# Performance work log

Hardware: AMD Instinct MI355X
Metric: run time of the kernel (lower is better)

## Reference

```python
import jax, jax.numpy as jnp
import numpy as np
import math

N_SLOTS, DIM, ITERS = 8, 256, 3
BATCH, TOKENS = 64, 4096


def _ln(x, g, b, eps=1e-5):
    mu = x.mean(-1, keepdims=True)
    var = ((x - mu) ** 2).mean(-1, keepdims=True)
    return (x - mu) * jax.lax.rsqrt(var + eps) * g + b


def setup_inputs() -> dict:
    key = jax.random.key(0)
    ks = jax.random.split(key, 16)
    d = DIM
    s = 0.02
    return {
        "inputs": jax.random.normal(ks[0], (BATCH, TOKENS, d), jnp.float32),
        "noise": jax.random.normal(ks[1], (BATCH, N_SLOTS, d), jnp.float32),
        "slots_mu": jax.random.normal(ks[2], (1, N_SLOTS, d), jnp.float32),
        "slots_logsigma": jnp.zeros((1, N_SLOTS, d), jnp.float32),
        "Wq": jax.random.normal(ks[3], (d, d), jnp.float32) * s,
        "Wk": jax.random.normal(ks[4], (d, d), jnp.float32) * s,
        "Wv": jax.random.normal(ks[5], (d, d), jnp.float32) * s,
        "W_ih": jax.random.normal(ks[6], (3 * d, d), jnp.float32) * s,
        "W_hh": jax.random.normal(ks[7], (3 * d, d), jnp.float32) * s,
        "b_ih": jnp.zeros((3 * d,), jnp.float32),
        "b_hh": jnp.zeros((3 * d,), jnp.float32),
        "mlp_W1": jax.random.normal(ks[8], (d, d), jnp.float32) * s,
        "mlp_b1": jnp.zeros((d,), jnp.float32),
        "mlp_W2": jax.random.normal(ks[9], (d, d), jnp.float32) * s,
        "mlp_b2": jnp.zeros((d,), jnp.float32),
        "ln_in_g": jnp.ones((d,), jnp.float32),
        "ln_in_b": jnp.zeros((d,), jnp.float32),
        "ln_slots_g": jnp.ones((d,), jnp.float32),
        "ln_slots_b": jnp.zeros((d,), jnp.float32),
        "ln_mlp_g": jnp.ones((d,), jnp.float32),
        "ln_mlp_b": jnp.zeros((d,), jnp.float32),
    }


def reference(inputs, noise, slots_mu, slots_logsigma, Wq, Wk, Wv,
              W_ih, W_hh, b_ih, b_hh, mlp_W1, mlp_b1, mlp_W2, mlp_b2,
              ln_in_g, ln_in_b, ln_slots_g, ln_slots_b, ln_mlp_g, ln_mlp_b):
    n, t, d = inputs.shape
    scale = 1.0 / math.sqrt(d)
    x = _ln(inputs, ln_in_g, ln_in_b)                      # [n,t,d]
    slots = slots_mu + jnp.exp(slots_logsigma) * noise     # [n,S,d]
    k = jnp.einsum('ntd,ed->nte', x, Wk)
    v = jnp.einsum('ntd,ed->nte', x, Wv)
    for _ in range(ITERS):
        slots_prev = slots
        q = jnp.einsum('nsd,ed->nse', _ln(slots, ln_slots_g, ln_slots_b), Wq)
        logits = jnp.einsum('nsd,ntd->nst', q, k) * scale  # [n,S,t]
        attn = jax.nn.softmax(logits, axis=-1)
        attn = attn / (attn.sum(-1, keepdims=True) + 1e-8)
        updates = jnp.einsum('nst,ntd->nsd', attn, v)      # [n,S,d]
        # GRUCell (torch gate order r,z,n)
        gi = jnp.einsum('nsd,ed->nse', updates, W_ih) + b_ih
        gh = jnp.einsum('nsd,ed->nse', slots_prev, W_hh) + b_hh
        gi_r, gi_z, gi_n = jnp.split(gi, 3, axis=-1)
        gh_r, gh_z, gh_n = jnp.split(gh, 3, axis=-1)
        r = jax.nn.sigmoid(gi_r + gh_r)
        z = jax.nn.sigmoid(gi_z + gh_z)
        h_new = jnp.tanh(gi_n + r * gh_n)
        slots = (1.0 - z) * h_new + z * slots_prev
        hid = jax.nn.relu(jnp.einsum('nsd,ed->nse', _ln(slots, ln_mlp_g, ln_mlp_b), mlp_W1) + mlp_b1)
        slots = slots + jnp.einsum('nsd,ed->nse', hid, mlp_W2) + mlp_b2
    return slots
```

## Files before the change

kernel.cpp:

```cpp
#include <hip/hip_runtime.h>
#include <math.h>

#define TOKENS 4096
#define BATCH 64

typedef __attribute__((ext_vector_type(8))) short bf16x8;
typedef __attribute__((ext_vector_type(4))) float f32x4;
union U4B { uint4 u; bf16x8 b; };
union U2x2B { uint2 u[2]; bf16x8 b; };

__device__ __forceinline__ float wsum(float v) {
#pragma unroll
  for (int m = 32; m >= 1; m >>= 1) v += __shfl_xor(v, m);
  return v;
}
__device__ __forceinline__ unsigned short f2bf(float f) {
  unsigned u = __float_as_uint(f);
  u += 0x7fffu + ((u >> 16) & 1u);
  return (unsigned short)(u >> 16);
}
__device__ __forceinline__ float bflo(unsigned p) { return __uint_as_float(p << 16); }
__device__ __forceinline__ float bfhi(unsigned p) { return __uint_as_float(p & 0xffff0000u); }
__device__ __forceinline__ float sigmf(float x) { return 1.f / (1.f + expf(-x)); }

__global__ __launch_bounds__(256) void k_pre(
    const float* __restrict__ in, const float* __restrict__ lin_g,
    const float* __restrict__ lin_b, unsigned* __restrict__ x,
    const float* __restrict__ Wq, const float* __restrict__ Wv,
    const float* __restrict__ Wih, const float* __restrict__ Whh,
    const float* __restrict__ W1, const float* __restrict__ W2,
    float* __restrict__ WqT, float* __restrict__ WvT, float* __restrict__ WihT,
    float* __restrict__ WhhT, float* __restrict__ W1T, float* __restrict__ W2T) {
  int bid = blockIdx.x, tid = threadIdx.x;
  if (bid < 65536) {
    int row = bid * 4 + (tid >> 6);
    int lane = tid & 63;
    const float* p = in + (size_t)row * 256 + lane * 4;
    float4 v = *(const float4*)p;
    float s  = wsum(v.x + v.y + v.z + v.w);
    float sq = wsum(v.x * v.x + v.y * v.y + v.z * v.z + v.w * v.w);
    float mu = s * (1.f / 256.f);
    float var = sq * (1.f / 256.f) - mu * mu;
    float rs = rsqrtf(var + 1e-5f);
    float4 gg = *(const float4*)(lin_g + lane * 4);
    float4 bb = *(const float4*)(lin_b + lane * 4);
    float y0 = (v.x - mu) * rs * gg.x + bb.x;
    float y1 = (v.y - mu) * rs * gg.y + bb.y;
    float y2 = (v.z - mu) * rs * gg.z + bb.z;
    float y3 = (v.w - mu) * rs * gg.w + bb.w;
    uint2 o;
    o.x = (unsigned)f2bf(y0) | ((unsigned)f2bf(y1) << 16);
    o.y = (unsigned)f2bf(y2) | ((unsigned)f2bf(y3) << 16);
    *(uint2*)(x + (size_t)row * 128 + lane * 2) = o;
    return;
  }
  {
    __shared__ float t[32][33];
    int t2 = bid - 65536;
    const float* S; float* D; int R; int tile;
    if (t2 < 64)       { S = Wq;  D = WqT;  R = 256; tile = t2; }
    else if (t2 < 128) { S = Wv;  D = WvT;  R = 256; tile = t2 - 64; }
    else if (t2 < 192) { S = W1;  D = W1T;  R = 256; tile = t2 - 128; }
    else if (t2 < 256) { S = W2;  D = W2T;  R = 256; tile = t2 - 192; }
    else if (t2 < 448) { S = Wih; D = WihT; R = 768; tile = t2 - 256; }
    else               { S = Whh; D = WhhT; R = 768; tile = t2 - 448; }
    int rt = R >> 5;
    int r0 = (tile % rt) * 32, c0 = (tile / rt) * 32;
    int ci = tid & 31, r8 = tid >> 5;
#pragma unroll
    for (int k = 0; k < 4; ++k) {
      int r = r8 + k * 8;
      t[r][ci] = S[(size_t)(r0 + r) * 256 + c0 + ci];
    }
    __syncthreads();
#pragma unroll
    for (int k = 0; k < 4; ++k) {
      int r = r8 + k * 8;
      D[(size_t)(c0 + r) * R + r0 + ci] = t[ci][r];
    }
  }
}

__global__ __launch_bounds__(256) void k_qw0(
    const float* __restrict__ smu, const float* __restrict__ slsig,
    const float* __restrict__ noise, const float* __restrict__ lsl_g,
    const float* __restrict__ lsl_b, const float* __restrict__ WqT,
    const float* __restrict__ Wk, float* __restrict__ slots,
    unsigned* __restrict__ qwb) {
  __shared__ float ln[256];
  __shared__ float q[256];
  __shared__ float red[8];
  int n = blockIdx.x, s = blockIdx.y, tid = threadIdx.x;
  int sd = s * 256 + tid;
  float v = smu[sd] + expf(slsig[sd]) * noise[(size_t)n * 2048 + sd];
  slots[(size_t)n * 2048 + sd] = v;
  float ps = wsum(v), pq = wsum(v * v);
  if ((tid & 63) == 0) { red[tid >> 6] = ps; red[4 + (tid >> 6)] = pq; }
  __syncthreads();
  float sum = red[0] + red[1] + red[2] + red[3];
  float sqq = red[4] + red[5] + red[6] + red[7];
  float mu = sum * (1.f / 256.f);
  float var = sqq * (1.f / 256.f) - mu * mu;
  float rs = rsqrtf(var + 1e-5f);
  ln[tid] = (v - mu) * rs * lsl_g[tid] + lsl_b[tid];
  __syncthreads();
  float a = 0.f;
  for (int d = 0; d < 256; ++d) a += ln[d] * WqT[d * 256 + tid];
  q[tid] = a;
  __syncthreads();
  float c = 0.f;
  for (int e = 0; e < 256; ++e) c += q[e] * Wk[(size_t)e * 256 + tid];
  c *= 0.0625f;
  __syncthreads();
  ln[tid] = c;
  __syncthreads();
  if (tid < 128)
    qwb[((size_t)n * 8 + s) * 128 + tid] =
        (unsigned)f2bf(ln[2 * tid]) | ((unsigned)f2bf(ln[2 * tid + 1]) << 16);
}

__global__ __launch_bounds__(256) void k_att(const unsigned* __restrict__ x,
                                             const unsigned* __restrict__ qwb,
                                             float2* __restrict__ stats,
                                             float* __restrict__ axp) {
  __shared__ unsigned xs[64][130];
  __shared__ float lsT[64][8];
  __shared__ float redM[8][4], redS[8][4];
  int ch = blockIdx.x, n = blockIdx.y;
  int tid = threadIdx.x, wv = tid >> 6, l = tid & 63;
  int col = l & 15, g = l >> 4;
  {
    int lane32 = tid & 31, g8 = tid >> 5;
    const unsigned* src = x + ((size_t)n * 4096 + ch * 64) * 128 + lane32 * 4;
#pragma unroll
    for (int p = 0; p < 8; ++p) {
      int row = p * 8 + g8;
      uint4 vv = *(const uint4*)(src + (size_t)row * 128);
      unsigned* dr = &xs[row][lane32 * 4];
      *(uint2*)dr = make_uint2(vv.x, vv.y);
      *(uint2*)(dr + 2) = make_uint2(vv.z, vv.w);
    }
  }
  uint4 a[8];
  {
    const unsigned* ap = qwb + ((size_t)n * 8 + (l & 7)) * 128 + g * 4;
#pragma unroll
    for (int kk = 0; kk < 8; ++kk) a[kk] = *(const uint4*)(ap + kk * 16);
  }
  __syncthreads();
  {
    int t0 = wv * 16;
    const unsigned* xr = &xs[t0 + col][0];
    f32x4 acc = {0.f, 0.f, 0.f, 0.f};
#pragma unroll
    for (int kk = 0; kk < 8; ++kk) {
      U4B aa;
      aa.u = a[kk];
      U2x2B bb;
      bb.u[0] = *(const uint2*)(xr + kk * 16 + g * 4);
      bb.u[1] = *(const uint2*)(xr + kk * 16 + g * 4 + 2);
      acc = __builtin_amdgcn_mfma_f32_16x16x32_bf16(aa.b, bb.b, acc, 0, 0, 0);
    }
    if (g < 2) {
#pragma unroll
      for (int r = 0; r < 4; ++r) lsT[t0 + col][g * 4 + r] = acc[r];
    }
  }
  __syncthreads();
  int s = tid & 7, tg = tid >> 3;
  float l0 = lsT[tg][s], l1 = lsT[tg + 32][s];
  {
    float M = fmaxf(l0, l1);
    M = fmaxf(M, __shfl_xor(M, 8));
    M = fmaxf(M, __shfl_xor(M, 16));
    M = fmaxf(M, __shfl_xor(M, 32));
    if ((tid & 63) < 8) redM[s][tid >> 6] = M;
  }
  __syncthreads();
  float Mf = fmaxf(fmaxf(redM[s][0], redM[s][1]), fmaxf(redM[s][2], redM[s][3]));
  {
    float e0 = expf(l0 - Mf), e1 = expf(l1 - Mf);
    lsT[tg][s] = e0;
    lsT[tg + 32][s] = e1;
    float S = e0 + e1;
    S += __shfl_xor(S, 8);
    S += __shfl_xor(S, 16);
    S += __shfl_xor(S, 32);
    if ((tid & 63) < 8) redS[s][tid >> 6] = S;
  }
  __syncthreads();
  if (tid < 8) {
    float M = fmaxf(fmaxf(redM[tid][0], redM[tid][1]), fmaxf(redM[tid][2], redM[tid][3]));
    float S = redS[tid][0] + redS[tid][1] + redS[tid][2] + redS[tid][3];
    stats[((size_t)n * 8 + tid) * 64 + ch] = make_float2(M, S);
  }
  {
    int d = tid;
    float acc[8] = {0, 0, 0, 0, 0, 0, 0, 0};
#pragma unroll 8
    for (int t = 0; t < 64; ++t) {
      unsigned pw = xs[t][d >> 1];
      float xv = (d & 1) ? bfhi(pw) : bflo(pw);
      float4 a0 = *(const float4*)&lsT[t][0];
      float4 a1 = *(const float4*)&lsT[t][4];
      acc[0] += a0.x * xv; acc[1] += a0.y * xv;
      acc[2] += a0.z * xv; acc[3] += a0.w * xv;
      acc[4] += a1.x * xv; acc[5] += a1.y * xv;
      acc[6] += a1.z * xv; acc[7] += a1.w * xv;
    }
    float* op = axp + (((size_t)n * 64 + ch) * 8) * 256 + d;
#pragma unroll
    for (int ss = 0; ss < 8; ++ss) op[ss * 256] = acc[ss];
  }
}

__global__ __launch_bounds__(512) void k_update3(
    const float* __restrict__ axp, const float2* __restrict__ stats,
    const float* __restrict__ slots_in,
    const float* __restrict__ WvT, const float* __restrict__ WihT,
    const float* __restrict__ WhhT, const float* __restrict__ b_ih,
    const float* __restrict__ b_hh, const float* __restrict__ W1T,
    const float* __restrict__ b1, const float* __restrict__ W2T,
    const float* __restrict__ b2, const float* __restrict__ lml_g,
    const float* __restrict__ lml_b, const float* __restrict__ lsl_g,
    const float* __restrict__ lsl_b, const float* __restrict__ WqT,
    const float* __restrict__ Wk, unsigned* __restrict__ qwb, int doQw,
    float* __restrict__ slots_out) {
  __shared__ float ax[4][256];
  __shared__ float sp[4][256];
  __shared__ float upd[4][256];
  __shared__ float gi[4][768];
  __shared__ float gh[4][768];
  __shared__ float sn[4][256];
  __shared__ float lnv[4][256];
  __shared__ float hid[4][256];
  __shared__ float red[16];
  __shared__ float wch[4][64];
  __shared__ float inv4[4];
  int n = blockIdx.x, sg = blockIdx.y * 4;
  int tid = threadIdx.x;
  if (tid < 4) {
    const float2* st = stats + ((size_t)n * 8 + sg + tid) * 64;
    float M = -3.4e38f;
#pragma unroll
    for (int c = 0; c < 64; ++c) M = fmaxf(M, st[c].x);
    float S = 0.f;
#pragma unroll
    for (int c = 0; c < 64; ++c) {
      float w = expf(st[c].x - M);
      wch[tid][c] = w;
      S += w * st[c].y;
    }
    inv4[tid] = 1.f / (S * (1.f + 1e-8f));
  }
  __syncthreads();
  for (int i = tid; i < 1024; i += 512) {
    int sl = i >> 8, d = i & 255;
    const float* pp = axp + ((size_t)n * 512 + sg + sl) * 256 + d;
    float a = 0.f;
#pragma unroll
    for (int c = 0; c < 64; ++c) a += wch[sl][c] * pp[(size_t)c * 2048];
    ax[sl][d] = a * inv4[sl];
    sp[sl][d] = slots_in[((size_t)n * 8 + sg + sl) * 256 + d];
  }
  __syncthreads();
  int e = tid & 255, h = tid >> 8;
  {
    float a0 = 0.f, a1 = 0.f;
    for (int d = 0; d < 256; ++d) {
      float w = WvT[d * 256 + e];
      a0 += ax[h * 2][d] * w;
      a1 += ax[h * 2 + 1][d] * w;
    }
    upd[h * 2][e] = a0;
    upd[h * 2 + 1][e] = a1;
  }
  __syncthreads();
  for (int jj = tid; jj < 1536; jj += 512) {
    bool ihs = jj < 768;
    int j = ihs ? jj : jj - 768;
    const float* WT = ihs ? WihT : WhhT;
    const float* src = ihs ? &upd[0][0] : &sp[0][0];
    float a0 = 0.f, a1 = 0.f, a2 = 0.f, a3 = 0.f;
    for (int d = 0; d < 256; ++d) {
      float w = WT[(size_t)d * 768 + j];
      a0 += src[d] * w;
      a1 += src[256 + d] * w;
      a2 += src[512 + d] * w;
      a3 += src[768 + d] * w;
    }
    float bb = ihs ? b_ih[j] : b_hh[j];
    float* dst = ihs ? &gi[0][0] : &gh[0][0];
    dst[j] = a0 + bb;
    dst[768 + j] = a1 + bb;
    dst[1536 + j] = a2 + bb;
    dst[2304 + j] = a3 + bb;
  }
  __syncthreads();
  for (int i = tid; i < 1024; i += 512) {
    int sl = i >> 8, j = i & 255;
    float r = sigmf(gi[sl][j] + gh[sl][j]);
    float z = sigmf(gi[sl][j + 256] + gh[sl][j + 256]);
    float hh = tanhf(gi[sl][j + 512] + r * gh[sl][j + 512]);
    sn[sl][j] = (1.f - z) * hh + z * sp[sl][j];
  }
  __syncthreads();
  {
    int sl = tid >> 7, qq = tid & 127;
    float v0 = sn[sl][qq], v1 = sn[sl][qq + 128];
    float ps = wsum(v0 + v1);
    float pq = wsum(v0 * v0 + v1 * v1);
    int wid = tid >> 6;
    if ((tid & 63) == 0) { red[wid] = ps; red[8 + wid] = pq; }
    __syncthreads();
    float ssum = red[sl * 2] + red[sl * 2 + 1];
    float sqq  = red[8 + sl * 2] + red[8 + sl * 2 + 1];
    float mu = ssum * (1.f / 256.f);
    float var = sqq * (1.f / 256.f) - mu * mu;
    float rs = rsqrtf(var + 1e-5f);
    lnv[sl][qq]       = (v0 - mu) * rs * lml_g[qq] + lml_b[qq];
    lnv[sl][qq + 128] = (v1 - mu) * rs * lml_g[qq + 128] + lml_b[qq + 128];
  }
  __syncthreads();
  {
    float a0 = 0.f, a1 = 0.f;
    for (int d = 0; d < 256; ++d) {
      float w = W1T[d * 256 + e];
      a0 += lnv[h * 2][d] * w;
      a1 += lnv[h * 2 + 1][d] * w;
    }
    hid[h * 2][e]     = fmaxf(a0 + b1[e], 0.f);
    hid[h * 2 + 1][e] = fmaxf(a1 + b1[e], 0.f);
  }
  __syncthreads();
  {
    float a0 = 0.f, a1 = 0.f;
    for (int d = 0; d < 256; ++d) {
      float w = W2T[d * 256 + e];
      a0 += hid[h * 2][d] * w;
      a1 += hid[h * 2 + 1][d] * w;
    }
    float o0 = sn[h * 2][e] + a0 + b2[e];
    float o1 = sn[h * 2 + 1][e] + a1 + b2[e];
    slots_out[((size_t)n * 8 + sg + h * 2) * 256 + e]     = o0;
    slots_out[((size_t)n * 8 + sg + h * 2 + 1) * 256 + e] = o1;
    ax[h * 2][e] = o0;
    ax[h * 2 + 1][e] = o1;
  }
  if (!doQw) return;
  __syncthreads();
  {
    int sl = tid >> 7, qq = tid & 127;
    float v0 = ax[sl][qq], v1 = ax[sl][qq + 128];
    float ps = wsum(v0 + v1);
    float pq = wsum(v0 * v0 + v1 * v1);
    int wid = tid >> 6;
    if ((tid & 63) == 0) { red[wid] = ps; red[8 + wid] = pq; }
    __syncthreads();
    float ssum = red[sl * 2] + red[sl * 2 + 1];
    float sqq  = red[8 + sl * 2] + red[8 + sl * 2 + 1];
    float mu = ssum * (1.f / 256.f);
    float var = sqq * (1.f / 256.f) - mu * mu;
    float rs = rsqrtf(var + 1e-5f);
    sp[sl][qq]       = (v0 - mu) * rs * lsl_g[qq] + lsl_b[qq];
    sp[sl][qq + 128] = (v1 - mu) * rs * lsl_g[qq + 128] + lsl_b[qq + 128];
  }
  __syncthreads();
  {
    float a0 = 0.f, a1 = 0.f;
    for (int d = 0; d < 256; ++d) {
      float w = WqT[d * 256 + e];
      a0 += sp[h * 2][d] * w;
      a1 += sp[h * 2 + 1][d] * w;
    }
    upd[h * 2][e] = a0;
    upd[h * 2 + 1][e] = a1;
  }
  __syncthreads();
  {
    float c0 = 0.f, c1 = 0.f;
    for (int ee = 0; ee < 256; ++ee) {
      float w = Wk[(size_t)ee * 256 + e];
      c0 += upd[h * 2][ee] * w;
      c1 += upd[h * 2 + 1][ee] * w;
    }
    hid[h * 2][e]     = c0 * 0.0625f;
    hid[h * 2 + 1][e] = c1 * 0.0625f;
  }
  __syncthreads();
  {
    int sl = tid >> 7, p = tid & 127;
    qwb[((size_t)n * 8 + sg + sl) * 128 + p] =
        (unsigned)f2bf(hid[sl][2 * p]) | ((unsigned)f2bf(hid[sl][2 * p + 1]) << 16);
  }
}

extern "C" void kernel_launch(void* const* d_in, const int* in_sizes, int n_in,
                              void* d_out, int out_size, void* d_ws, size_t ws_size,
                              hipStream_t stream) {
  (void)in_sizes; (void)n_in; (void)out_size; (void)ws_size;
  const float* inputs = (const float*)d_in[0];
  const float* noise  = (const float*)d_in[1];
  const float* smu    = (const float*)d_in[2];
  const float* slsig  = (const float*)d_in[3];
  const float* Wq     = (const float*)d_in[4];
  const float* Wk     = (const float*)d_in[5];
  const float* Wv     = (const float*)d_in[6];
  const float* W_ih   = (const float*)d_in[7];
  const float* W_hh   = (const float*)d_in[8];
  const float* b_ih   = (const float*)d_in[9];
  const float* b_hh   = (const float*)d_in[10];
  const float* W1     = (const float*)d_in[11];
  const float* b1     = (const float*)d_in[12];
  const float* W2     = (const float*)d_in[13];
  const float* b2     = (const float*)d_in[14];
  const float* lin_g  = (const float*)d_in[15];
  const float* lin_b  = (const float*)d_in[16];
  const float* lsl_g  = (const float*)d_in[17];
  const float* lsl_b  = (const float*)d_in[18];
  const float* lml_g  = (const float*)d_in[19];
  const float* lml_b  = (const float*)d_in[20];
  float* out = (float*)d_out;
  char* ws = (char*)d_ws;
  unsigned* x    = (unsigned*)(ws + 0);
  unsigned* qwb  = (unsigned*)(ws + 134217728);
  float2* stats  = (float2*)(ws + 134479872);
  float* axp     = (float*)(ws + 134742016);
  float* WqT     = (float*)(ws + 168296448);
  float* WvT     = (float*)(ws + 168558592);
  float* WihT    = (float*)(ws + 168820736);
  float* WhhT    = (float*)(ws + 169607168);
  float* W1T     = (float*)(ws + 170393600);
  float* W2T     = (float*)(ws + 170655744);

  k_pre<<<dim3(66176), 256, 0, stream>>>(inputs, lin_g, lin_b, x,
                                         Wq, Wv, W_ih, W_hh, W1, W2,
                                         WqT, WvT, WihT, WhhT, W1T, W2T);
  k_qw0<<<dim3(BATCH, 8), 256, 0, stream>>>(smu, slsig, noise, lsl_g, lsl_b,
                                            WqT, Wk, out, qwb);
  for (int it = 0; it < 3; ++it) {
    k_att<<<dim3(64, BATCH), 256, 0, stream>>>(x, qwb, stats, axp);
    k_update3<<<dim3(BATCH, 2), 512, 0, stream>>>(
        axp, stats, out, WvT, WihT, WhhT, b_ih, b_hh, W1T, b1, W2T, b2,
        lml_g, lml_b, lsl_g, lsl_b, WqT, Wk, qwb, (it < 2) ? 1 : 0, out);
  }
}
```

Baseline: 463.5 us.

## Process four token chunks per attention block with online softmax and register prefetch

Each attention block now walks 256 tokens in four 64-token chunks instead of one chunk. It keeps a running max and sum per slot, as in online softmax, and prefetches the next chunk into registers while the current one is being computed. This cuts the per-chunk partial outputs and stats by four, which shrinks the axp workspace and the reduction work in k_update3. In exchange there are more barriers per block and only 1024 blocks instead of 4096, which may lower occupancy and latency hiding.

```diff
diff --git a/kernel.cpp b/kernel.cpp
--- a/kernel.cpp
+++ b/kernel.cpp
@@ -126,89 +126,123 @@
   __shared__ unsigned xs[64][130];
   __shared__ float lsT[64][8];
   __shared__ float redM[8][4], redS[8][4];
-  int ch = blockIdx.x, n = blockIdx.y;
+  __shared__ float Mrun[8], Srun[8], scl[8], Mnew[8];
+  int bk = blockIdx.x, n = blockIdx.y;
   int tid = threadIdx.x, wv = tid >> 6, l = tid & 63;
   int col = l & 15, g = l >> 4;
-  {
-    int lane32 = tid & 31, g8 = tid >> 5;
-    const unsigned* src = x + ((size_t)n * 4096 + ch * 64) * 128 + lane32 * 4;
-#pragma unroll
-    for (int p = 0; p < 8; ++p) {
-      int row = p * 8 + g8;
-      uint4 vv = *(const uint4*)(src + (size_t)row * 128);
-      unsigned* dr = &xs[row][lane32 * 4];
-      *(uint2*)dr = make_uint2(vv.x, vv.y);
-      *(uint2*)(dr + 2) = make_uint2(vv.z, vv.w);
-    }
-  }
   uint4 a[8];
   {
     const unsigned* ap = qwb + ((size_t)n * 8 + (l & 7)) * 128 + g * 4;
 #pragma unroll
     for (int kk = 0; kk < 8; ++kk) a[kk] = *(const uint4*)(ap + kk * 16);
   }
-  __syncthreads();
-  {
-    int t0 = wv * 16;
-    const unsigned* xr = &xs[t0 + col][0];
-    f32x4 acc = {0.f, 0.f, 0.f, 0.f};
-#pragma unroll
-    for (int kk = 0; kk < 8; ++kk) {
-      U4B aa;
-      aa.u = a[kk];
-      U2x2B bb;
-      bb.u[0] = *(const uint2*)(xr + kk * 16 + g * 4);
-      bb.u[1] = *(const uint2*)(xr + kk * 16 + g * 4 + 2);
-      acc = __builtin_amdgcn_mfma_f32_16x16x32_bf16(aa.b, bb.b, acc, 0, 0, 0);
-    }
-    if (g < 2) {
-#pragma unroll
-      for (int r = 0; r < 4; ++r) lsT[t0 + col][g * 4 + r] = acc[r];
-    }
+  if (tid < 8) { Mrun[tid] = -3.4e38f; Srun[tid] = 0.f; }
+  float acc[8] = {0, 0, 0, 0, 0, 0, 0, 0};
+  int lane32 = tid & 31, g8 = tid >> 5;
+  const unsigned* base = x + ((size_t)n * 4096 + bk * 256) * 128 + lane32 * 4;
+  uint4 st[8];
+#pragma unroll
+  for (int p = 0; p < 8; ++p)
+    st[p] = *(const uint4*)(base + (size_t)(p * 8 + g8) * 128);
+#pragma unroll
+  for (int p = 0; p < 8; ++p) {
+    unsigned* dr = &xs[p * 8 + g8][lane32 * 4];
+    *(uint2*)dr = make_uint2(st[p].x, st[p].y);
+    *(uint2*)(dr + 2) = make_uint2(st[p].z, st[p].w);
   }
   __syncthreads();
   int s = tid & 7, tg = tid >> 3;
-  float l0 = lsT[tg][s], l1 = lsT[tg + 32][s];
-  {
-    float M = fmaxf(l0, l1);
-    M = fmaxf(M, __shfl_xor(M, 8));
-    M = fmaxf(M, __shfl_xor(M, 16));
-    M = fmaxf(M, __shfl_xor(M, 32));
-    if ((tid & 63) < 8) redM[s][tid >> 6] = M;
-  }
-  __syncthreads();
-  float Mf = fmaxf(fmaxf(redM[s][0], redM[s][1]), fmaxf(redM[s][2], redM[s][3]));
-  {
-    float e0 = expf(l0 - Mf), e1 = expf(l1 - Mf);
-    lsT[tg][s] = e0;
-    lsT[tg + 32][s] = e1;
-    float S = e0 + e1;
-    S += __shfl_xor(S, 8);
-    S += __shfl_xor(S, 16);
-    S += __shfl_xor(S, 32);
-    if ((tid & 63) < 8) redS[s][tid >> 6] = S;
-  }
-  __syncthreads();
-  if (tid < 8) {
-    float M = fmaxf(fmaxf(redM[tid][0], redM[tid][1]), fmaxf(redM[tid][2], redM[tid][3]));
-    float S = redS[tid][0] + redS[tid][1] + redS[tid][2] + redS[tid][3];
-    stats[((size_t)n * 8 + tid) * 64 + ch] = make_float2(M, S);
-  }
-  {
-    int d = tid;
-    float acc[8] = {0, 0, 0, 0, 0, 0, 0, 0};
+  for (int c = 0; c < 4; ++c) {
+    if (c < 3) {
+      const unsigned* src = base + (size_t)(c + 1) * 64 * 128;
+#pragma unroll
+      for (int p = 0; p < 8; ++p)
+        st[p] = *(const uint4*)(src + (size_t)(p * 8 + g8) * 128);
+    }
+    {
+      int t0 = wv * 16;
+      const unsigned* xr = &xs[t0 + col][0];
+      f32x4 qacc = {0.f, 0.f, 0.f, 0.f};
+#pragma unroll
+      for (int kk = 0; kk < 8; ++kk) {
+        U4B aa; aa.u = a[kk];
+        U2x2B bb;
+        bb.u[0] = *(const uint2*)(xr + kk * 16 + g * 4);
+        bb.u[1] = *(const uint2*)(xr + kk * 16 + g * 4 + 2);
+        qacc = __builtin_amdgcn_mfma_f32_16x16x32_bf16(aa.b, bb.b, qacc, 0, 0, 0);
+      }
+      if (g < 2) {
+#pragma unroll
+        for (int r = 0; r < 4; ++r) lsT[t0 + col][g * 4 + r] = qacc[r];
+      }
+    }
+    __syncthreads();
+    float l0 = lsT[tg][s], l1 = lsT[tg + 32][s];
+    {
+      float M = fmaxf(l0, l1);
+      M = fmaxf(M, __shfl_xor(M, 8));
+      M = fmaxf(M, __shfl_xor(M, 16));
+      M = fmaxf(M, __shfl_xor(M, 32));
+      if (l < 8) redM[s][wv] = M;
+    }
+    __syncthreads();
+    if (tid < 8) {
+      float Mc = fmaxf(fmaxf(redM[tid][0], redM[tid][1]),
+                       fmaxf(redM[tid][2], redM[tid][3]));
+      float Mn = fmaxf(Mrun[tid], Mc);
+      scl[tid] = expf(Mrun[tid] - Mn);
+      Mnew[tid] = Mn;
+      Mrun[tid] = Mn;
+    }
+    __syncthreads();
+    {
+      float Mn = Mnew[s];
+      float e0 = expf(l0 - Mn), e1 = expf(l1 - Mn);
+      lsT[tg][s] = e0;
+      lsT[tg + 32][s] = e1;
+      float S = e0 + e1;
+      S += __shfl_xor(S, 8);
+      S += __shfl_xor(S, 16);
+      S += __shfl_xor(S, 32);
+      if (l < 8) redS[s][wv] = S;
+    }
+    __syncthreads();
+    if (tid < 8) {
+      float Sc = redS[tid][0] + redS[tid][1] + redS[tid][2] + redS[tid][3];
+      Srun[tid] = Srun[tid] * scl[tid] + Sc;
+    }
+    {
+      int d = tid;
+      float pv[8] = {0, 0, 0, 0, 0, 0, 0, 0};
 #pragma unroll 8
-    for (int t = 0; t < 64; ++t) {
-      unsigned pw = xs[t][d >> 1];
-      float xv = (d & 1) ? bfhi(pw) : bflo(pw);
-      float4 a0 = *(const float4*)&lsT[t][0];
-      float4 a1 = *(const float4*)&lsT[t][4];
-      acc[0] += a0.x * xv; acc[1] += a0.y * xv;
-      acc[2] += a0.z * xv; acc[3] += a0.w * xv;
-      acc[4] += a1.x * xv; acc[5] += a1.y * xv;
-      acc[6] += a1.z * xv; acc[7] += a1.w * xv;
-    }
-    float* op = axp + (((size_t)n * 64 + ch) * 8) * 256 + d;
+      for (int t = 0; t < 64; ++t) {
+        unsigned pw = xs[t][d >> 1];
+        float xv = (d & 1) ? bfhi(pw) : bflo(pw);
+        float4 a0 = *(const float4*)&lsT[t][0];
+        float4 a1 = *(const float4*)&lsT[t][4];
+        pv[0] += a0.x * xv; pv[1] += a0.y * xv;
+        pv[2] += a0.z * xv; pv[3] += a0.w * xv;
+        pv[4] += a1.x * xv; pv[5] += a1.y * xv;
+        pv[6] += a1.z * xv; pv[7] += a1.w * xv;
+      }
+#pragma unroll
+      for (int ss = 0; ss < 8; ++ss) acc[ss] = acc[ss] * scl[ss] + pv[ss];
+    }
+    __syncthreads();
+    if (c < 3) {
+#pragma unroll
+      for (int p = 0; p < 8; ++p) {
+        unsigned* dr = &xs[p * 8 + g8][lane32 * 4];
+        *(uint2*)dr = make_uint2(st[p].x, st[p].y);
+        *(uint2*)(dr + 2) = make_uint2(st[p].z, st[p].w);
+      }
+      __syncthreads();
+    }
+  }
+  if (tid < 8)
+    stats[((size_t)n * 8 + tid) * 16 + bk] = make_float2(Mrun[tid], Srun[tid]);
+  {
+    float* op = axp + (((size_t)n * 16 + bk) * 8) * 256 + tid;
 #pragma unroll
     for (int ss = 0; ss < 8; ++ss) op[ss * 256] = acc[ss];
   }
@@ -235,18 +269,18 @@
   __shared__ float lnv[4][256];
   __shared__ float hid[4][256];
   __shared__ float red[16];
-  __shared__ float wch[4][64];
+  __shared__ float wch[4][16];
   __shared__ float inv4[4];
   int n = blockIdx.x, sg = blockIdx.y * 4;
   int tid = threadIdx.x;
   if (tid < 4) {
-    const float2* st = stats + ((size_t)n * 8 + sg + tid) * 64;
+    const float2* st = stats + ((size_t)n * 8 + sg + tid) * 16;
     float M = -3.4e38f;
 #pragma unroll
-    for (int c = 0; c < 64; ++c) M = fmaxf(M, st[c].x);
+    for (int c = 0; c < 16; ++c) M = fmaxf(M, st[c].x);
     float S = 0.f;
 #pragma unroll
-    for (int c = 0; c < 64; ++c) {
+    for (int c = 0; c < 16; ++c) {
       float w = expf(st[c].x - M);
       wch[tid][c] = w;
       S += w * st[c].y;
@@ -256,10 +290,10 @@
   __syncthreads();
   for (int i = tid; i < 1024; i += 512) {
     int sl = i >> 8, d = i & 255;
-    const float* pp = axp + ((size_t)n * 512 + sg + sl) * 256 + d;
+    const float* pp = axp + (size_t)n * 32768 + (sg + sl) * 256 + d;
     float a = 0.f;
 #pragma unroll
-    for (int c = 0; c < 64; ++c) a += wch[sl][c] * pp[(size_t)c * 2048];
+    for (int c = 0; c < 16; ++c) a += wch[sl][c] * pp[(size_t)c * 2048];
     ax[sl][d] = a * inv4[sl];
     sp[sl][d] = slots_in[((size_t)n * 8 + sg + sl) * 256 + d];
   }
@@ -425,13 +459,13 @@
   unsigned* x    = (unsigned*)(ws + 0);
   unsigned* qwb  = (unsigned*)(ws + 134217728);
   float2* stats  = (float2*)(ws + 134479872);
-  float* axp     = (float*)(ws + 134742016);
-  float* WqT     = (float*)(ws + 168296448);
-  float* WvT     = (float*)(ws + 168558592);
-  float* WihT    = (float*)(ws + 168820736);
-  float* WhhT    = (float*)(ws + 169607168);
-  float* W1T     = (float*)(ws + 170393600);
-  float* W2T     = (float*)(ws + 170655744);
+  float* axp     = (float*)(ws + 134545408);
+  float* WqT     = (float*)(ws + 142934016);
+  float* WvT     = (float*)(ws + 143196160);
+  float* WihT    = (float*)(ws + 143458304);
+  float* WhhT    = (float*)(ws + 144244736);
+  float* W1T     = (float*)(ws + 145031168);
+  float* W2T     = (float*)(ws + 145293312);
 
   k_pre<<<dim3(66176), 256, 0, stream>>>(inputs, lin_g, lin_b, x,
                                          Wq, Wv, W_ih, W_hh, W1, W2,
@@ -439,7 +473,7 @@
   k_qw0<<<dim3(BATCH, 8), 256, 0, stream>>>(smu, slsig, noise, lsl_g, lsl_b,
                                             WqT, Wk, out, qwb);
   for (int it = 0; it < 3; ++it) {
-    k_att<<<dim3(64, BATCH), 256, 0, stream>>>(x, qwb, stats, axp);
+    k_att<<<dim3(16, BATCH), 256, 0, stream>>>(x, qwb, stats, axp);
     k_update3<<<dim3(BATCH, 2), 512, 0, stream>>>(
         axp, stats, out, WvT, WihT, WhhT, b_ih, b_hh, W1T, b1, W2T, b2,
         lml_g, lml_b, lsl_g, lsl_b, WqT, Wk, qwb, (it < 2) ? 1 : 0, out);
```

Result: slower. 496.1 us (+7.0%).
